# Kernel tuning notes

Measured on AMD Instinct MI355X. Metric: run time of the kernel, lower is better.

## Reference

```python
import jax, jax.numpy as jnp
import numpy as np

B, S, F, D, H, L, NSUB, DFF = 64, 128, 62, 256, 4, 6, 32, 512
DH = D // 2           # each attention branch works on half of d_model
DEPTH = DH // H       # per-head dim = 32
NEG = -1000000000.0


def _rescale(w):
    # (1+e) / (1+exp(1-w))
    e1 = jnp.exp(jnp.float32(1.0))
    return (1.0 + e1) / (1.0 + jnp.exp(1.0 - w))


def _ln(x, g, b):
    mu = jnp.mean(x, -1, keepdims=True)
    v = jnp.var(x, -1, keepdims=True)
    return (x - mu) / jnp.sqrt(v + 1e-6) * g + b


def _heads(x, W, b):
    bsz, s, _ = x.shape
    return (x @ W + b).reshape(bsz, s, H, DEPTH).transpose(0, 2, 1, 3)  # (B,H,S,depth)


def setup_inputs():
    key = jax.random.key(0)
    ks = list(jax.random.split(key, 16))
    it = iter(ks)
    n = lambda shape: jax.random.normal(next(it), shape, jnp.float32) * 0.02
    inp = {
        "x": jax.random.normal(next(it), (B, S, F), jnp.float32),
        "adj_matrix": jax.random.normal(next(it), (B, S, S), jnp.float32),
        "dist_matrix": jax.random.uniform(next(it), (B, S, S), jnp.float32) * 10.0,
        "atom_match_matrix": jax.random.uniform(next(it), (B, NSUB, S), jnp.float32),
        "sum_atoms": jnp.ones((B, NSUB, 1), jnp.float32),
        "emb_W": n((F, D)), "emb_b": jnp.zeros((D,), jnp.float32),
        "glob_W": n((D, D)), "glob_b": jnp.zeros((D,), jnp.float32),
    }
    # per-layer params, stacked along leading L axis for lax.scan
    for p in ["Wq1", "Wk1", "Wv1", "Wo1", "Wq2", "Wk2", "Wv2", "Wo2"]:
        inp[p] = n((L, DH, DH))
    for p in ["bq1", "bk1", "bv1", "bo1", "bq2", "bk2", "bv2", "bo2"]:
        inp[p] = jnp.zeros((L, DH), jnp.float32)
    inp["Wf1"] = n((L, D, DFF)); inp["bf1"] = jnp.zeros((L, DFF), jnp.float32)
    inp["Wf2"] = n((L, DFF, D)); inp["bf2"] = jnp.zeros((L, D), jnp.float32)
    inp["g1"] = jnp.ones((L, D), jnp.float32); inp["be1"] = jnp.zeros((L, D), jnp.float32)
    inp["g2"] = jnp.ones((L, D), jnp.float32); inp["be2"] = jnp.zeros((L, D), jnp.float32)
    return inp


def reference(x, adj_matrix, dist_matrix, atom_match_matrix, sum_atoms,
              emb_W, emb_b, glob_W, glob_b,
              Wq1, Wk1, Wv1, Wo1, Wq2, Wk2, Wv2, Wo2,
              bq1, bk1, bv1, bo1, bq2, bk2, bv2, bo2,
              Wf1, bf1, Wf2, bf2, g1, be1, g2, be2):
    # padding mask from raw atom features: (B,1,1,S)
    mask = (jnp.sum(x, -1) == 0).astype(jnp.float32)[:, None, None, :]
    adj = adj_matrix[:, None]                  # (B,1,S,S) additive bias
    dist = _rescale(dist_matrix)[:, None]      # (B,1,S,S) multiplicative bias
    scale = 1.0 / jnp.sqrt(jnp.float32(DEPTH))

    h = jax.nn.relu(x @ emb_W + emb_b)         # embedding (eval mode, no dropout)

    def layer(h, p):
        (wq1, wk1, wv1, wo1, wq2, wk2, wv2, wo2,
         bq1_, bk1_, bv1_, bo1_, bq2_, bk2_, bv2_, bo2_,
         wf1, bf1_, wf2, bf2_, gg1, bb1, gg2, bb2) = p
        x1, x2 = jnp.split(h, 2, axis=-1)
        # local branch: plain scaled dot product + mask + adjacency bias
        Q = _heads(x1, wq1, bq1_); K = _heads(x1, wk1, bk1_); V = _heads(x1, wv1, bv1_)
        s = jnp.einsum('bhid,bhjd->bhij', Q, K) * scale + mask * NEG + adj
        o = jnp.einsum('bhij,bhjd->bhid', jax.nn.softmax(s, -1), V)
        x_l = o.transpose(0, 2, 1, 3).reshape(h.shape[0], S, DH) @ wo1 + bo1_
        # global branch: relu(QK^T) * rescaled_dist * scale + mask
        Q = _heads(x2, wq2, bq2_); K = _heads(x2, wk2, bk2_); V = _heads(x2, wv2, bv2_)
        s = jax.nn.relu(jnp.einsum('bhid,bhjd->bhij', Q, K)) * dist * scale + mask * NEG
        o = jnp.einsum('bhij,bhjd->bhid', jax.nn.softmax(s, -1), V)
        x_g = o.transpose(0, 2, 1, 3).reshape(h.shape[0], S, DH) @ wo2 + bo2_
        attn = jnp.concatenate([x_l, x_g], -1)
        out1 = _ln(h + attn, gg1, bb1)
        ffn = jax.nn.gelu(out1 @ wf1 + bf1_, approximate=False) @ wf2 + bf2_
        return _ln(ffn + out1, gg2, bb2), None

    xs = (Wq1, Wk1, Wv1, Wo1, Wq2, Wk2, Wv2, Wo2,
          bq1, bk1, bv1, bo1, bq2, bk2, bv2, bo2,
          Wf1, bf1, Wf2, bf2, g1, be1, g2, be2)
    h, _ = jax.lax.scan(layer, h, xs)

    pooled = (atom_match_matrix @ h) / sum_atoms      # (B,NSUB,D)
    out = jax.nn.relu(pooled @ glob_W + glob_b)
    return out
```

## Files before the change

kernel.cpp:

```cpp
#include <hip/hip_runtime.h>
#include <math.h>

#define B_ 64
#define S_ 128
#define F_ 62
#define D_ 256
#define H_ 4
#define L_ 6
#define NSUB_ 32
#define DFF_ 512
#define DH_ 128
#define DEPTH_ 32
#define MS_ (B_*S_)
#define NEGV (-1000000000.0f)
#define SCALE_ 0.17677669529663687f

typedef unsigned short u16;
typedef __attribute__((ext_vector_type(8))) short short8;
typedef __attribute__((ext_vector_type(4))) float f32x4;

__device__ __forceinline__ u16 f2b(float f){
  unsigned u = __float_as_uint(f);
  unsigned r = (u + 0x7fffu + ((u >> 16) & 1u)) >> 16;
  return (u16)r;
}

__device__ __forceinline__ void glds16(const void* g, void* l){
  __builtin_amdgcn_global_load_lds(
      (const __attribute__((address_space(1))) unsigned int*)g,
      (__attribute__((address_space(3))) unsigned int*)l, 16, 0, 0);
}

__global__ __launch_bounds__(256) void adjrescale_kernel(
    const float* __restrict__ adj, const float* __restrict__ dist,
    const float* __restrict__ maskb,
    float* __restrict__ adjm, float* __restrict__ distr){
  size_t i = (size_t)blockIdx.x*256 + threadIdx.x;
  int j = (int)(i & (S_-1));
  int b = (int)(i >> 14);
  const float e1 = 2.718281828459045f;
  distr[i] = (1.0f + e1) / (1.0f + expf(1.0f - dist[i])) * SCALE_;
  adjm[i]  = adj[i] + maskb[b*S_ + j];
}

struct TD { const float* src; u16* dst; int K, N, L; };
struct TDs { TD d[11]; };
__global__ __launch_bounds__(256) void transpose_all_kernel(TDs a){
  const TD p = a.d[blockIdx.z];
  int n0 = blockIdx.x*32, k0 = blockIdx.y*32;
  if(n0 >= p.N || k0 >= p.K) return;
  __shared__ float tbuf[32][33];
  int tx = threadIdx.x, ty = threadIdx.y;
  for(int l = 0; l < p.L; l++){
    const float* src = p.src + (size_t)l*p.K*p.N;
    u16* dst = p.dst + (size_t)l*p.K*p.N;
    #pragma unroll
    for(int i = 0; i < 4; i++)
      tbuf[ty + i*8][tx] = src[(size_t)(k0 + ty + i*8)*p.N + n0 + tx];
    __syncthreads();
    #pragma unroll
    for(int i = 0; i < 4; i++)
      dst[(size_t)(n0 + ty + i*8)*p.K + k0 + tx] = f2b(tbuf[tx][ty + i*8]);
    __syncthreads();
  }
}

__global__ __launch_bounds__(256) void embed_kernel(const float* __restrict__ x,
    const float* __restrict__ W, const float* __restrict__ bias,
    float* __restrict__ h, u16* __restrict__ h_bf, float* __restrict__ maskb){
  __shared__ float xs[4][F_];
  int r0 = blockIdx.x*4;
  int t = threadIdx.x;
  if(t < 4*F_){ int rr = t / F_, ff = t - rr*F_; xs[rr][ff] = x[(size_t)(r0+rr)*F_ + ff]; }
  __syncthreads();
  if(t < 4){
    float s = 0.f;
    #pragma unroll
    for(int f = 0; f < F_; f++) s += xs[t][f];
    maskb[r0 + t] = (s == 0.0f) ? NEGV : 0.0f;
  }
  float b = bias[t];
  float a0=b, a1=b, a2=b, a3=b;
  for(int k=0; k<F_; k++){
    float w = W[k*D_ + t];
    a0 = fmaf(xs[0][k], w, a0);
    a1 = fmaf(xs[1][k], w, a1);
    a2 = fmaf(xs[2][k], w, a2);
    a3 = fmaf(xs[3][k], w, a3);
  }
  a0 = fmaxf(a0, 0.f); a1 = fmaxf(a1, 0.f); a2 = fmaxf(a2, 0.f); a3 = fmaxf(a3, 0.f);
  h[(size_t)(r0+0)*D_ + t] = a0;  h_bf[(size_t)(r0+0)*D_ + t] = f2b(a0);
  h[(size_t)(r0+1)*D_ + t] = a1;  h_bf[(size_t)(r0+1)*D_ + t] = f2b(a1);
  h[(size_t)(r0+2)*D_ + t] = a2;  h_bf[(size_t)(r0+2)*D_ + t] = f2b(a2);
  h[(size_t)(r0+3)*D_ + t] = a3;  h_bf[(size_t)(r0+3)*D_ + t] = f2b(a3);
}

struct MG {
  const u16* A; const u16* W; const float* bias; void* C;
  int lda, K, ldc, aofs, cofs;
};
struct MG6 { MG g[6]; };

template<int TM, bool OUTBF, int ACT>
__global__ __launch_bounds__(256) void mgemm_kernel(MG6 args){
  const MG p = args.g[blockIdx.z];
  __shared__ u16 As[TM*32];
  __shared__ u16 Bs[128*32];
  const int t    = threadIdx.x;
  const int lane = t & 63;
  const int w    = t >> 6;
  const int ln   = lane & 15;
  const int qd   = lane >> 4;
  const int mw   = (w & 1) * (TM/2);
  const int nw   = (w >> 1) * 64;
  const int m0   = blockIdx.x * TM;
  const int n0   = blockIdx.y * 128;
  constexpr int MI = TM/32;
  f32x4 acc[MI][4];
  #pragma unroll
  for(int i=0;i<MI;i++)
    #pragma unroll
    for(int j=0;j<4;j++) acc[i][j] = (f32x4){0.f,0.f,0.f,0.f};

  const int srow = t >> 2;
  const int sc8  = (t & 3) * 8;

  for(int k0 = 0; k0 < p.K; k0 += 32){
    __syncthreads();
    glds16(p.A + (size_t)(m0 + srow)*p.lda + p.aofs + k0 + sc8, As + t*8);
    if(TM == 128)
      glds16(p.A + (size_t)(m0 + 64 + srow)*p.lda + p.aofs + k0 + sc8, As + (t+256)*8);
    glds16(p.W + (size_t)(n0 + srow)*p.K + k0 + sc8, Bs + t*8);
    glds16(p.W + (size_t)(n0 + 64 + srow)*p.K + k0 + sc8, Bs + (t+256)*8);
    __syncthreads();

    short8 a[MI], b[4];
    #pragma unroll
    for(int i=0;i<MI;i++) a[i] = *(const short8*)&As[(mw + i*16 + ln)*32 + qd*8];
    #pragma unroll
    for(int j=0;j<4;j++)  b[j] = *(const short8*)&Bs[(nw + j*16 + ln)*32 + qd*8];
    #pragma unroll
    for(int i=0;i<MI;i++)
      #pragma unroll
      for(int j=0;j<4;j++)
        acc[i][j] = __builtin_amdgcn_mfma_f32_16x16x32_bf16(a[i], b[j], acc[i][j], 0, 0, 0);
  }

  #pragma unroll
  for(int i=0;i<MI;i++){
    #pragma unroll
    for(int j=0;j<4;j++){
      int col = n0 + nw + j*16 + ln;
      float bv = p.bias[col];
      int rowb = m0 + mw + i*16 + qd*4;
      #pragma unroll
      for(int r=0;r<4;r++){
        float v = acc[i][j][r] + bv;
        if(ACT == 1) v = fmaxf(v, 0.f);
        if(ACT == 2) v = 0.5f*v*(1.0f + erff(v*0.70710678118654752f));
        size_t idx = (size_t)(rowb + r)*p.ldc + p.cofs + col;
        if(OUTBF) ((u16*)p.C)[idx] = f2b(v);
        else      ((float*)p.C)[idx] = v;
      }
    }
  }
}

struct QAArgs { const u16 *wq, *wk, *wv; const float *bq, *bk, *bv; };

__global__ __launch_bounds__(256) void qkv_attn_kernel(
    const u16* __restrict__ h_bf,
    QAArgs a1, QAArgs a2,
    const float* __restrict__ adjm, const float* __restrict__ distr,
    const float* __restrict__ maskb,
    u16* __restrict__ o1, u16* __restrict__ o2)
{
  __shared__ u16 SH[21760];
  u16* As = SH;
  u16* Bs = SH + 4096;
  u16* Qs = SH + 7168;
  u16* Ks = SH + 12288;
  u16* Vt = SH + 17408;
  u16* Ps = SH;

  const int bh = blockIdx.x;
  const int b  = bh >> 2;
  const int hh = bh & 3;
  const int branch = blockIdx.y;
  const QAArgs qa = branch ? a2 : a1;
  const u16* wqp = qa.wq + (size_t)hh*32*DH_;
  const u16* wkp = qa.wk + (size_t)hh*32*DH_;
  const u16* wvp = qa.wv + (size_t)hh*32*DH_;
  const int t = threadIdx.x;
  const int w = t >> 6, lane = t & 63;
  const int ln = lane & 15, qd = lane >> 4;
  const size_t rowbase = (size_t)b * S_;
  const int srow = t >> 2, sc8 = (t & 3) * 8;

  f32x4 acc[2][6];
  #pragma unroll
  for(int i=0;i<2;i++)
    #pragma unroll
    for(int j=0;j<6;j++) acc[i][j] = (f32x4){0.f,0.f,0.f,0.f};

  for(int k0 = 0; k0 < DH_; k0 += 32){
    __syncthreads();
    glds16(h_bf + (rowbase + srow)*D_ + branch*DH_ + k0 + sc8, As + t*8);
    glds16(h_bf + (rowbase + 64 + srow)*D_ + branch*DH_ + k0 + sc8, As + (t+256)*8);
    {
      int r = t >> 2;
      const u16* wp = (r < 32) ? wqp : wkp;
      glds16(wp + (size_t)(r & 31)*DH_ + k0 + sc8, Bs + t*8);
    }
    if(t < 128){
      int c = 256 + t;
      glds16(wvp + (size_t)((c>>2) - 64)*DH_ + k0 + (c&3)*8, Bs + c*8);
    }
    __syncthreads();
    short8 av[2];
    #pragma unroll
    for(int mt = 0; mt < 2; mt++)
      av[mt] = *(const short8*)&As[(w*32 + mt*16 + ln)*32 + qd*8];
    #pragma unroll
    for(int nt = 0; nt < 6; nt++){
      short8 bv = *(const short8*)&Bs[(nt*16 + ln)*32 + qd*8];
      #pragma unroll
      for(int mt = 0; mt < 2; mt++)
        acc[mt][nt] = __builtin_amdgcn_mfma_f32_16x16x32_bf16(av[mt], bv, acc[mt][nt], 0, 0, 0);
    }
  }

  {
    const float* bqp = qa.bq + hh*32;
    const float* bkp = qa.bk + hh*32;
    const float* bvp = qa.bv + hh*32;
    #pragma unroll
    for(int mt = 0; mt < 2; mt++){
      int rb = w*32 + mt*16 + qd*4;
      #pragma unroll
      for(int j = 0; j < 2; j++){
        int d = j*16 + ln;
        float bq_ = bqp[d], bk_ = bkp[d], bv_ = bvp[d];
        #pragma unroll
        for(int r = 0; r < 4; r++){
          Qs[(rb+r)*40 + d]   = f2b(acc[mt][j][r]   + bq_);
          Ks[(rb+r)*40 + d]   = f2b(acc[mt][2+j][r] + bk_);
          Vt[d*136 + rb + r]  = f2b(acc[mt][4+j][r] + bv_);
        }
      }
    }
  }
  __syncthreads();

  const int mbase = w * 32;
  short8 qf[2];
  #pragma unroll
  for(int mt = 0; mt < 2; mt++)
    qf[mt] = *(const short8*)&Qs[(mbase + mt*16 + ln)*40 + qd*8];
  short8 kf[8];
  #pragma unroll
  for(int nt = 0; nt < 8; nt++)
    kf[nt] = *(const short8*)&Ks[(nt*16 + ln)*40 + qd*8];
  __syncthreads();

  f32x4 sc[2][8];
  #pragma unroll
  for(int mt = 0; mt < 2; mt++)
    #pragma unroll
    for(int nt = 0; nt < 8; nt++)
      sc[mt][nt] = __builtin_amdgcn_mfma_f32_16x16x32_bf16(
          qf[mt], kf[nt], (f32x4){0.f,0.f,0.f,0.f}, 0, 0, 0);

  float mskv[8];
  if(branch){
    #pragma unroll
    for(int nt = 0; nt < 8; nt++) mskv[nt] = maskb[rowbase + nt*16 + ln];
  }

  #pragma unroll
  for(int mt = 0; mt < 2; mt++){
    #pragma unroll
    for(int r = 0; r < 4; r++){
      int row = mbase + mt*16 + qd*4 + r;
      const float* arow = (branch ? distr : adjm) + (rowbase + row)*S_ + ln;
      #pragma unroll
      for(int nt = 0; nt < 8; nt++){
        float g = arow[nt*16];
        float v;
        if(branch == 0) v = sc[mt][nt][r]*SCALE_ + g;
        else            v = fmaxf(sc[mt][nt][r], 0.f)*g + mskv[nt];
        sc[mt][nt][r] = v;
      }
    }
  }

  #pragma unroll
  for(int mt = 0; mt < 2; mt++){
    #pragma unroll
    for(int r = 0; r < 4; r++){
      float m = -3.4e38f;
      #pragma unroll
      for(int nt = 0; nt < 8; nt++) m = fmaxf(m, sc[mt][nt][r]);
      m = fmaxf(m, __shfl_xor(m, 1));
      m = fmaxf(m, __shfl_xor(m, 2));
      m = fmaxf(m, __shfl_xor(m, 4));
      m = fmaxf(m, __shfl_xor(m, 8));
      float sum = 0.f;
      float e[8];
      #pragma unroll
      for(int nt = 0; nt < 8; nt++){ e[nt] = __expf(sc[mt][nt][r] - m); sum += e[nt]; }
      sum += __shfl_xor(sum, 1);
      sum += __shfl_xor(sum, 2);
      sum += __shfl_xor(sum, 4);
      sum += __shfl_xor(sum, 8);
      float inv = 1.0f / sum;
      int row = mbase + mt*16 + qd*4 + r;
      #pragma unroll
      for(int nt = 0; nt < 8; nt++) Ps[row*136 + nt*16 + ln] = f2b(e[nt] * inv);
    }
  }

  f32x4 oacc[2][2];
  #pragma unroll
  for(int mt = 0; mt < 2; mt++)
    #pragma unroll
    for(int n2 = 0; n2 < 2; n2++) oacc[mt][n2] = (f32x4){0.f,0.f,0.f,0.f};
  #pragma unroll
  for(int kk = 0; kk < 4; kk++){
    short8 pa[2], vb[2];
    #pragma unroll
    for(int mt = 0; mt < 2; mt++)
      pa[mt] = *(const short8*)&Ps[(mbase + mt*16 + ln)*136 + kk*32 + qd*8];
    #pragma unroll
    for(int n2 = 0; n2 < 2; n2++)
      vb[n2] = *(const short8*)&Vt[(n2*16 + ln)*136 + kk*32 + qd*8];
    #pragma unroll
    for(int mt = 0; mt < 2; mt++)
      #pragma unroll
      for(int n2 = 0; n2 < 2; n2++)
        oacc[mt][n2] = __builtin_amdgcn_mfma_f32_16x16x32_bf16(pa[mt], vb[n2], oacc[mt][n2], 0, 0, 0);
  }

  u16* Og = branch ? o2 : o1;
  #pragma unroll
  for(int mt = 0; mt < 2; mt++){
    #pragma unroll
    for(int n2 = 0; n2 < 2; n2++){
      #pragma unroll
      for(int r = 0; r < 4; r++){
        int row = mbase + mt*16 + qd*4 + r;
        int d   = n2*16 + ln;
        Og[(rowbase + row)*DH_ + hh*DEPTH_ + d] = f2b(oacc[mt][n2][r]);
      }
    }
  }
}

__global__ __launch_bounds__(128) void oproj_ln_kernel(
    const u16* __restrict__ o1, const u16* __restrict__ o2,
    const u16* __restrict__ w1, const u16* __restrict__ w2,
    const float* __restrict__ b1, const float* __restrict__ b2,
    const float* __restrict__ hres,
    const float* __restrict__ g, const float* __restrict__ be,
    float* __restrict__ out, u16* __restrict__ outb)
{
  __shared__ u16 As1[32*32], As2[32*32], Bs1[128*32], Bs2[128*32];
  __shared__ float biasv[256], gs[256], bes[256];
  const int t = threadIdx.x;
  const int lane = t & 63, w = t >> 6;
  const int ln = lane & 15, qd = lane >> 4;
  const int m0 = blockIdx.x * 32;
  biasv[t] = b1[t & 127]; biasv[128 + t] = b2[t & 127];
  gs[t] = g[t]; gs[128+t] = g[128+t];
  bes[t] = be[t]; bes[128+t] = be[128+t];
  const int sc8 = (t & 3) * 8;
  f32x4 acc[16];
  #pragma unroll
  for(int i=0;i<16;i++) acc[i] = (f32x4){0.f,0.f,0.f,0.f};

  for(int k0 = 0; k0 < DH_; k0 += 32){
    __syncthreads();
    glds16(o1 + (size_t)(m0 + (t>>2))*DH_ + k0 + sc8, As1 + t*8);
    glds16(o2 + (size_t)(m0 + (t>>2))*DH_ + k0 + sc8, As2 + t*8);
    #pragma unroll
    for(int j = 0; j < 4; j++){
      int c = t + 128*j;
      glds16(w1 + (size_t)(c>>2)*DH_ + k0 + sc8, Bs1 + c*8);
      glds16(w2 + (size_t)(c>>2)*DH_ + k0 + sc8, Bs2 + c*8);
    }
    __syncthreads();
    short8 a1 = *(const short8*)&As1[(w*16+ln)*32 + qd*8];
    short8 a2 = *(const short8*)&As2[(w*16+ln)*32 + qd*8];
    #pragma unroll
    for(int nt = 0; nt < 8; nt++){
      short8 bv = *(const short8*)&Bs1[(nt*16+ln)*32 + qd*8];
      acc[nt] = __builtin_amdgcn_mfma_f32_16x16x32_bf16(a1, bv, acc[nt], 0, 0, 0);
    }
    #pragma unroll
    for(int nt = 0; nt < 8; nt++){
      short8 bv = *(const short8*)&Bs2[(nt*16+ln)*32 + qd*8];
      acc[8+nt] = __builtin_amdgcn_mfma_f32_16x16x32_bf16(a2, bv, acc[8+nt], 0, 0, 0);
    }
  }

  const int rb = m0 + w*16 + qd*4;
  float mu[4] = {0,0,0,0};
  #pragma unroll
  for(int nt = 0; nt < 16; nt++){
    int col = nt*16 + ln;
    float bv = biasv[col];
    #pragma unroll
    for(int r = 0; r < 4; r++){
      float v = acc[nt][r] + bv + hres[(size_t)(rb+r)*D_ + col];
      acc[nt][r] = v;
      mu[r] += v;
    }
  }
  #pragma unroll
  for(int r = 0; r < 4; r++){
    float s = mu[r];
    s += __shfl_xor(s,1); s += __shfl_xor(s,2); s += __shfl_xor(s,4); s += __shfl_xor(s,8);
    mu[r] = s * (1.0f/D_);
  }
  float iv[4] = {0,0,0,0};
  #pragma unroll
  for(int nt = 0; nt < 16; nt++)
    #pragma unroll
    for(int r = 0; r < 4; r++){ float d = acc[nt][r] - mu[r]; iv[r] += d*d; }
  #pragma unroll
  for(int r = 0; r < 4; r++){
    float s = iv[r];
    s += __shfl_xor(s,1); s += __shfl_xor(s,2); s += __shfl_xor(s,4); s += __shfl_xor(s,8);
    iv[r] = rsqrtf(s*(1.0f/D_) + 1e-6f);
  }
  #pragma unroll
  for(int nt = 0; nt < 16; nt++){
    int col = nt*16 + ln;
    float gg = gs[col], bb = bes[col];
    #pragma unroll
    for(int r = 0; r < 4; r++){
      float y = (acc[nt][r] - mu[r])*iv[r]*gg + bb;
      size_t idx = (size_t)(rb+r)*D_ + col;
      out[idx] = y;
      outb[idx] = f2b(y);
    }
  }
}

__global__ __launch_bounds__(128) void ffn2_ln_kernel(
    const u16* __restrict__ A, const u16* __restrict__ W,
    const float* __restrict__ bias,
    const float* __restrict__ res,
    const float* __restrict__ g, const float* __restrict__ be,
    float* __restrict__ out, u16* __restrict__ outb)
{
  __shared__ u16 As[32*32], Bs[256*32];
  __shared__ float biasv[256], gs[256], bes[256];
  const int t = threadIdx.x;
  const int lane = t & 63, w = t >> 6;
  const int ln = lane & 15, qd = lane >> 4;
  const int m0 = blockIdx.x * 32;
  biasv[t] = bias[t]; biasv[128+t] = bias[128+t];
  gs[t] = g[t]; gs[128+t] = g[128+t];
  bes[t] = be[t]; bes[128+t] = be[128+t];
  const int sc8 = (t & 3) * 8;
  f32x4 acc[16];
  #pragma unroll
  for(int i=0;i<16;i++) acc[i] = (f32x4){0.f,0.f,0.f,0.f};

  for(int k0 = 0; k0 < DFF_; k0 += 32){
    __syncthreads();
    glds16(A + (size_t)(m0 + (t>>2))*DFF_ + k0 + sc8, As + t*8);
    #pragma unroll
    for(int j = 0; j < 8; j++){
      int c = t + 128*j;
      glds16(W + (size_t)(c>>2)*DFF_ + k0 + sc8, Bs + c*8);
    }
    __syncthreads();
    short8 a = *(const short8*)&As[(w*16+ln)*32 + qd*8];
    #pragma unroll
    for(int nt = 0; nt < 16; nt++){
      short8 bv = *(const short8*)&Bs[(nt*16+ln)*32 + qd*8];
      acc[nt] = __builtin_amdgcn_mfma_f32_16x16x32_bf16(a, bv, acc[nt], 0, 0, 0);
    }
  }

  const int rb = m0 + w*16 + qd*4;
  float mu[4] = {0,0,0,0};
  #pragma unroll
  for(int nt = 0; nt < 16; nt++){
    int col = nt*16 + ln;
    float bv = biasv[col];
    #pragma unroll
    for(int r = 0; r < 4; r++){
      float v = acc[nt][r] + bv + res[(size_t)(rb+r)*D_ + col];
      acc[nt][r] = v;
      mu[r] += v;
    }
  }
  #pragma unroll
  for(int r = 0; r < 4; r++){
    float s = mu[r];
    s += __shfl_xor(s,1); s += __shfl_xor(s,2); s += __shfl_xor(s,4); s += __shfl_xor(s,8);
    mu[r] = s * (1.0f/D_);
  }
  float iv[4] = {0,0,0,0};
  #pragma unroll
  for(int nt = 0; nt < 16; nt++)
    #pragma unroll
    for(int r = 0; r < 4; r++){ float d = acc[nt][r] - mu[r]; iv[r] += d*d; }
  #pragma unroll
  for(int r = 0; r < 4; r++){
    float s = iv[r];
    s += __shfl_xor(s,1); s += __shfl_xor(s,2); s += __shfl_xor(s,4); s += __shfl_xor(s,8);
    iv[r] = rsqrtf(s*(1.0f/D_) + 1e-6f);
  }
  #pragma unroll
  for(int nt = 0; nt < 16; nt++){
    int col = nt*16 + ln;
    float gg = gs[col], bb = bes[col];
    #pragma unroll
    for(int r = 0; r < 4; r++){
      float y = (acc[nt][r] - mu[r])*iv[r]*gg + bb;
      size_t idx = (size_t)(rb+r)*D_ + col;
      out[idx] = y;
      outb[idx] = f2b(y);
    }
  }
}

__global__ __launch_bounds__(256) void pool_kernel(
    const float* __restrict__ amm, const float* __restrict__ sum_atoms,
    const float* __restrict__ h, u16* __restrict__ pooled_bf)
{
  __shared__ float as[S_];
  int bn = blockIdx.x;
  int b  = bn >> 5;
  int t  = threadIdx.x;
  if(t < S_) as[t] = amm[(size_t)bn*S_ + t];
  __syncthreads();
  float acc = 0.f;
  const float* hb = h + (size_t)b*S_*D_ + t;
  #pragma unroll 4
  for(int s = 0; s < S_; s++) acc = fmaf(as[s], hb[(size_t)s*D_], acc);
  pooled_bf[(size_t)bn*D_ + t] = f2b(acc / sum_atoms[bn]);
}

extern "C" void kernel_launch(void* const* d_in, const int* in_sizes, int n_in,
                              void* d_out, int out_size, void* d_ws, size_t ws_size,
                              hipStream_t stream)
{
  const float* x     = (const float*)d_in[0];
  const float* adj   = (const float*)d_in[1];
  const float* dist  = (const float*)d_in[2];
  const float* amm   = (const float*)d_in[3];
  const float* sum_a = (const float*)d_in[4];
  const float* embW  = (const float*)d_in[5];
  const float* embB  = (const float*)d_in[6];
  const float* globW = (const float*)d_in[7];
  const float* globB = (const float*)d_in[8];
  const float* Wq1 = (const float*)d_in[9],  *Wk1 = (const float*)d_in[10],
             *Wv1 = (const float*)d_in[11], *Wo1 = (const float*)d_in[12],
             *Wq2 = (const float*)d_in[13], *Wk2 = (const float*)d_in[14],
             *Wv2 = (const float*)d_in[15], *Wo2 = (const float*)d_in[16];
  const float* bq1 = (const float*)d_in[17], *bk1 = (const float*)d_in[18],
             *bv1 = (const float*)d_in[19], *bo1 = (const float*)d_in[20],
             *bq2 = (const float*)d_in[21], *bk2 = (const float*)d_in[22],
             *bv2 = (const float*)d_in[23], *bo2 = (const float*)d_in[24];
  const float* Wf1 = (const float*)d_in[25], *bf1 = (const float*)d_in[26],
             *Wf2 = (const float*)d_in[27], *bf2 = (const float*)d_in[28],
             *g1  = (const float*)d_in[29], *be1 = (const float*)d_in[30],
             *g2  = (const float*)d_in[31], *be2 = (const float*)d_in[32];

  float* wsf = (float*)d_ws;
  float* h     = wsf; wsf += (size_t)MS_*D_;
  float* maskb = wsf; wsf += MS_;
  float* distr = wsf; wsf += (size_t)B_*S_*S_;
  float* adjm  = wsf; wsf += (size_t)B_*S_*S_;
  float* slab  = wsf; wsf += (size_t)MS_*DH_*8;
  float* out1  = wsf; wsf += (size_t)MS_*D_;
  u16* bb = (u16*)wsf;
  u16* h_bf    = bb; bb += (size_t)MS_*D_;
  u16* out1_bf = bb; bb += (size_t)MS_*D_;
  u16* pooled_bf = bb; bb += (size_t)B_*NSUB_*D_;
  u16* globWt  = bb; bb += (size_t)D_*D_;
  u16* wq1t = bb; bb += (size_t)L_*DH_*DH_;
  u16* wk1t = bb; bb += (size_t)L_*DH_*DH_;
  u16* wv1t = bb; bb += (size_t)L_*DH_*DH_;
  u16* wo1t = bb; bb += (size_t)L_*DH_*DH_;
  u16* wq2t = bb; bb += (size_t)L_*DH_*DH_;
  u16* wk2t = bb; bb += (size_t)L_*DH_*DH_;
  u16* wv2t = bb; bb += (size_t)L_*DH_*DH_;
  u16* wo2t = bb; bb += (size_t)L_*DH_*DH_;
  u16* wf1t = bb; bb += (size_t)L_*D_*DFF_;
  u16* wf2t = bb; bb += (size_t)L_*DFF_*D_;
  u16* ffn1_bf = (u16*)slab;
  u16* o1_bf   = (u16*)slab + (size_t)MS_*DH_*6;
  u16* o2_bf   = (u16*)slab + (size_t)MS_*DH_*7;

  embed_kernel<<<MS_/4, 256, 0, stream>>>(x, embW, embB, h, h_bf, maskb);
  adjrescale_kernel<<<(B_*S_*S_)/256, 256, 0, stream>>>(adj, dist, maskb, adjm, distr);
  {
    TDs td;
    const float* S8[8] = {Wq1, Wk1, Wv1, Wo1, Wq2, Wk2, Wv2, Wo2};
    u16* D8[8] = {wq1t, wk1t, wv1t, wo1t, wq2t, wk2t, wv2t, wo2t};
    for(int i = 0; i < 8; i++) td.d[i] = {S8[i], D8[i], DH_, DH_, L_};
    td.d[8]  = {Wf1, wf1t, D_, DFF_, L_};
    td.d[9]  = {Wf2, wf2t, DFF_, D_, L_};
    td.d[10] = {globW, globWt, D_, D_, 1};
    transpose_all_kernel<<<dim3(16,16,11), dim3(32,8), 0, stream>>>(td);
  }

  for(int l = 0; l < L_; l++){
    QAArgs a1 = { wq1t + (size_t)l*DH_*DH_, wk1t + (size_t)l*DH_*DH_, wv1t + (size_t)l*DH_*DH_,
                  bq1 + (size_t)l*DH_, bk1 + (size_t)l*DH_, bv1 + (size_t)l*DH_ };
    QAArgs a2 = { wq2t + (size_t)l*DH_*DH_, wk2t + (size_t)l*DH_*DH_, wv2t + (size_t)l*DH_*DH_,
                  bq2 + (size_t)l*DH_, bk2 + (size_t)l*DH_, bv2 + (size_t)l*DH_ };
    qkv_attn_kernel<<<dim3(B_*H_, 2), 256, 0, stream>>>(h_bf, a1, a2, adjm, distr, maskb,
                                                        o1_bf, o2_bf);
    oproj_ln_kernel<<<MS_/32, 128, 0, stream>>>(
        o1_bf, o2_bf,
        wo1t + (size_t)l*DH_*DH_, wo2t + (size_t)l*DH_*DH_,
        bo1 + (size_t)l*DH_, bo2 + (size_t)l*DH_,
        h, g1 + (size_t)l*D_, be1 + (size_t)l*D_,
        out1, out1_bf);
    {
      MG6 a;
      a.g[0].A = out1_bf; a.g[0].W = wf1t + (size_t)l*D_*DFF_;
      a.g[0].bias = bf1 + (size_t)l*DFF_; a.g[0].C = ffn1_bf;
      a.g[0].lda = D_; a.g[0].K = D_; a.g[0].ldc = DFF_;
      a.g[0].aofs = 0; a.g[0].cofs = 0;
      mgemm_kernel<64,true,2><<<dim3(MS_/64, DFF_/128, 1), 256, 0, stream>>>(a);
    }
    ffn2_ln_kernel<<<MS_/32, 128, 0, stream>>>(
        ffn1_bf, wf2t + (size_t)l*DFF_*D_,
        bf2 + (size_t)l*D_,
        out1, g2 + (size_t)l*D_, be2 + (size_t)l*D_,
        h, h_bf);
  }

  pool_kernel<<<B_*NSUB_, 256, 0, stream>>>(amm, sum_a, h, pooled_bf);
  {
    MG6 a;
    a.g[0].A = pooled_bf; a.g[0].W = globWt;
    a.g[0].bias = globB; a.g[0].C = (float*)d_out;
    a.g[0].lda = D_; a.g[0].K = D_; a.g[0].ldc = D_;
    a.g[0].aofs = 0; a.g[0].cofs = 0;
    mgemm_kernel<64,false,1><<<dim3((B_*NSUB_)/64, D_/128, 1), 256, 0, stream>>>(a);
  }
}
```

Baseline: 475.1 us.

## Fuse output projection, LN1, FFN1+GELU, FFN2 and LN2 into one tail kernel

Replaces the per-layer oproj_ln, FFN1 GEMM and ffn2_ln launches with a single 256-thread kernel per 32-row tile. The LN1 output and GELU intermediate stay in shared memory instead of round-tripping through global buffers. Weights are now read straight from global memory as MFMA fragments rather than staged through LDS. Each block now rereads the full FFN weights, and LayerNorm switches to a one-pass sum/sum-of-squares variance, which is slightly less numerically robust.

```diff
diff --git a/kernel.cpp b/kernel.cpp
--- a/kernel.cpp
+++ b/kernel.cpp
@@ -356,175 +356,223 @@
   }
 }
 
-__global__ __launch_bounds__(128) void oproj_ln_kernel(
-    const u16* __restrict__ o1, const u16* __restrict__ o2,
-    const u16* __restrict__ w1, const u16* __restrict__ w2,
-    const float* __restrict__ b1, const float* __restrict__ b2,
-    const float* __restrict__ hres,
-    const float* __restrict__ g, const float* __restrict__ be,
-    float* __restrict__ out, u16* __restrict__ outb)
-{
-  __shared__ u16 As1[32*32], As2[32*32], Bs1[128*32], Bs2[128*32];
-  __shared__ float biasv[256], gs[256], bes[256];
+struct TailArgs {
+  const u16 *o1, *o2, *wo1, *wo2, *w1, *w2;
+  const float *bo1, *bo2, *bf1, *bf2, *g1, *be1, *g2, *be2;
+  float *h; u16 *h_bf;
+};
+
+__global__ __launch_bounds__(256) void tail_kernel(TailArgs p){
+  __shared__ u16 X1[32*264];
+  __shared__ u16 X2[32*520];
+  __shared__ float redS[4][32], redQ[4][32];
   const int t = threadIdx.x;
-  const int lane = t & 63, w = t >> 6;
+  const int w = t >> 6, lane = t & 63;
   const int ln = lane & 15, qd = lane >> 4;
   const int m0 = blockIdx.x * 32;
-  biasv[t] = b1[t & 127]; biasv[128 + t] = b2[t & 127];
-  gs[t] = g[t]; gs[128+t] = g[128+t];
-  bes[t] = be[t]; bes[128+t] = be[128+t];
-  const int sc8 = (t & 3) * 8;
-  f32x4 acc[16];
-  #pragma unroll
-  for(int i=0;i<16;i++) acc[i] = (f32x4){0.f,0.f,0.f,0.f};
-
+  const int branch = w >> 1;
+  const int c0 = w * 64;
+  const int bc0 = (w & 1) * 64;
+
+  const u16* Ao = branch ? p.o2 : p.o1;
+  const u16* Wo = branch ? p.wo2 : p.wo1;
+  const float* bo = branch ? p.bo2 : p.bo1;
+  f32x4 y[2][4];
+  #pragma unroll
+  for(int mt=0;mt<2;mt++)
+    #pragma unroll
+    for(int nt=0;nt<4;nt++) y[mt][nt] = (f32x4){0.f,0.f,0.f,0.f};
+
+  #pragma unroll
   for(int k0 = 0; k0 < DH_; k0 += 32){
-    __syncthreads();
-    glds16(o1 + (size_t)(m0 + (t>>2))*DH_ + k0 + sc8, As1 + t*8);
-    glds16(o2 + (size_t)(m0 + (t>>2))*DH_ + k0 + sc8, As2 + t*8);
-    #pragma unroll
-    for(int j = 0; j < 4; j++){
-      int c = t + 128*j;
-      glds16(w1 + (size_t)(c>>2)*DH_ + k0 + sc8, Bs1 + c*8);
-      glds16(w2 + (size_t)(c>>2)*DH_ + k0 + sc8, Bs2 + c*8);
-    }
-    __syncthreads();
-    short8 a1 = *(const short8*)&As1[(w*16+ln)*32 + qd*8];
-    short8 a2 = *(const short8*)&As2[(w*16+ln)*32 + qd*8];
-    #pragma unroll
-    for(int nt = 0; nt < 8; nt++){
-      short8 bv = *(const short8*)&Bs1[(nt*16+ln)*32 + qd*8];
-      acc[nt] = __builtin_amdgcn_mfma_f32_16x16x32_bf16(a1, bv, acc[nt], 0, 0, 0);
-    }
-    #pragma unroll
-    for(int nt = 0; nt < 8; nt++){
-      short8 bv = *(const short8*)&Bs2[(nt*16+ln)*32 + qd*8];
-      acc[8+nt] = __builtin_amdgcn_mfma_f32_16x16x32_bf16(a2, bv, acc[8+nt], 0, 0, 0);
-    }
-  }
-
-  const int rb = m0 + w*16 + qd*4;
-  float mu[4] = {0,0,0,0};
-  #pragma unroll
-  for(int nt = 0; nt < 16; nt++){
-    int col = nt*16 + ln;
-    float bv = biasv[col];
-    #pragma unroll
-    for(int r = 0; r < 4; r++){
-      float v = acc[nt][r] + bv + hres[(size_t)(rb+r)*D_ + col];
-      acc[nt][r] = v;
-      mu[r] += v;
-    }
-  }
-  #pragma unroll
-  for(int r = 0; r < 4; r++){
-    float s = mu[r];
-    s += __shfl_xor(s,1); s += __shfl_xor(s,2); s += __shfl_xor(s,4); s += __shfl_xor(s,8);
-    mu[r] = s * (1.0f/D_);
-  }
-  float iv[4] = {0,0,0,0};
-  #pragma unroll
-  for(int nt = 0; nt < 16; nt++)
-    #pragma unroll
-    for(int r = 0; r < 4; r++){ float d = acc[nt][r] - mu[r]; iv[r] += d*d; }
-  #pragma unroll
-  for(int r = 0; r < 4; r++){
-    float s = iv[r];
-    s += __shfl_xor(s,1); s += __shfl_xor(s,2); s += __shfl_xor(s,4); s += __shfl_xor(s,8);
-    iv[r] = rsqrtf(s*(1.0f/D_) + 1e-6f);
-  }
-  #pragma unroll
-  for(int nt = 0; nt < 16; nt++){
-    int col = nt*16 + ln;
-    float gg = gs[col], bb = bes[col];
-    #pragma unroll
-    for(int r = 0; r < 4; r++){
-      float y = (acc[nt][r] - mu[r])*iv[r]*gg + bb;
-      size_t idx = (size_t)(rb+r)*D_ + col;
-      out[idx] = y;
-      outb[idx] = f2b(y);
-    }
-  }
-}
-
-__global__ __launch_bounds__(128) void ffn2_ln_kernel(
-    const u16* __restrict__ A, const u16* __restrict__ W,
-    const float* __restrict__ bias,
-    const float* __restrict__ res,
-    const float* __restrict__ g, const float* __restrict__ be,
-    float* __restrict__ out, u16* __restrict__ outb)
-{
-  __shared__ u16 As[32*32], Bs[256*32];
-  __shared__ float biasv[256], gs[256], bes[256];
-  const int t = threadIdx.x;
-  const int lane = t & 63, w = t >> 6;
-  const int ln = lane & 15, qd = lane >> 4;
-  const int m0 = blockIdx.x * 32;
-  biasv[t] = bias[t]; biasv[128+t] = bias[128+t];
-  gs[t] = g[t]; gs[128+t] = g[128+t];
-  bes[t] = be[t]; bes[128+t] = be[128+t];
-  const int sc8 = (t & 3) * 8;
-  f32x4 acc[16];
-  #pragma unroll
-  for(int i=0;i<16;i++) acc[i] = (f32x4){0.f,0.f,0.f,0.f};
-
+    short8 af[2], bf[4];
+    #pragma unroll
+    for(int mt=0;mt<2;mt++)
+      af[mt] = *(const short8*)(Ao + (size_t)(m0+mt*16+ln)*DH_ + k0 + qd*8);
+    #pragma unroll
+    for(int nt=0;nt<4;nt++)
+      bf[nt] = *(const short8*)(Wo + (size_t)(bc0+nt*16+ln)*DH_ + k0 + qd*8);
+    #pragma unroll
+    for(int mt=0;mt<2;mt++)
+      #pragma unroll
+      for(int nt=0;nt<4;nt++)
+        y[mt][nt] = __builtin_amdgcn_mfma_f32_16x16x32_bf16(af[mt], bf[nt], y[mt][nt], 0, 0, 0);
+  }
+
+  float sS[2][4] = {}, sQ[2][4] = {};
+  #pragma unroll
+  for(int mt=0;mt<2;mt++){
+    #pragma unroll
+    for(int nt=0;nt<4;nt++){
+      int col = c0 + nt*16 + ln;
+      float bv = bo[bc0 + nt*16 + ln];
+      #pragma unroll
+      for(int r=0;r<4;r++){
+        float v = y[mt][nt][r] + bv + p.h[(size_t)(m0+mt*16+qd*4+r)*D_ + col];
+        y[mt][nt][r] = v;
+        sS[mt][r] += v;
+        sQ[mt][r] += v*v;
+      }
+    }
+  }
+  #pragma unroll
+  for(int mt=0;mt<2;mt++)
+    #pragma unroll
+    for(int r=0;r<4;r++){
+      float a = sS[mt][r], b = sQ[mt][r];
+      a += __shfl_xor(a,1); a += __shfl_xor(a,2); a += __shfl_xor(a,4); a += __shfl_xor(a,8);
+      b += __shfl_xor(b,1); b += __shfl_xor(b,2); b += __shfl_xor(b,4); b += __shfl_xor(b,8);
+      sS[mt][r] = a; sQ[mt][r] = b;
+    }
+  if(ln == 0){
+    #pragma unroll
+    for(int mt=0;mt<2;mt++)
+      #pragma unroll
+      for(int r=0;r<4;r++){
+        int row = mt*16 + qd*4 + r;
+        redS[w][row] = sS[mt][r];
+        redQ[w][row] = sQ[mt][r];
+      }
+  }
+  __syncthreads();
+  float mu[2][4], iv[2][4];
+  #pragma unroll
+  for(int mt=0;mt<2;mt++)
+    #pragma unroll
+    for(int r=0;r<4;r++){
+      int row = mt*16 + qd*4 + r;
+      float s = redS[0][row] + redS[1][row] + redS[2][row] + redS[3][row];
+      float q = redQ[0][row] + redQ[1][row] + redQ[2][row] + redQ[3][row];
+      float m_ = s * (1.0f/D_);
+      mu[mt][r] = m_;
+      iv[mt][r] = rsqrtf(q*(1.0f/D_) - m_*m_ + 1e-6f);
+    }
+  #pragma unroll
+  for(int mt=0;mt<2;mt++){
+    #pragma unroll
+    for(int nt=0;nt<4;nt++){
+      int col = c0 + nt*16 + ln;
+      float gg = p.g1[col], bb = p.be1[col];
+      #pragma unroll
+      for(int r=0;r<4;r++){
+        float yy = (y[mt][nt][r] - mu[mt][r]) * iv[mt][r] * gg + bb;
+        y[mt][nt][r] = yy;
+        X1[(mt*16+qd*4+r)*264 + col] = f2b(yy);
+      }
+    }
+  }
+  __syncthreads();
+
+  {
+    const int fc0 = w * 128;
+    f32x4 f1[2][8];
+    #pragma unroll
+    for(int mt=0;mt<2;mt++)
+      #pragma unroll
+      for(int nt=0;nt<8;nt++) f1[mt][nt] = (f32x4){0.f,0.f,0.f,0.f};
+    for(int k0 = 0; k0 < D_; k0 += 32){
+      short8 a0 = *(const short8*)&X1[(ln)*264 + k0 + qd*8];
+      short8 a1 = *(const short8*)&X1[(16+ln)*264 + k0 + qd*8];
+      #pragma unroll
+      for(int nt=0;nt<8;nt++){
+        short8 bfr = *(const short8*)(p.w1 + (size_t)(fc0+nt*16+ln)*D_ + k0 + qd*8);
+        f1[0][nt] = __builtin_amdgcn_mfma_f32_16x16x32_bf16(a0, bfr, f1[0][nt], 0, 0, 0);
+        f1[1][nt] = __builtin_amdgcn_mfma_f32_16x16x32_bf16(a1, bfr, f1[1][nt], 0, 0, 0);
+      }
+    }
+    #pragma unroll
+    for(int mt=0;mt<2;mt++){
+      #pragma unroll
+      for(int nt=0;nt<8;nt++){
+        int col = fc0 + nt*16 + ln;
+        float bv = p.bf1[col];
+        #pragma unroll
+        for(int r=0;r<4;r++){
+          float v = f1[mt][nt][r] + bv;
+          v = 0.5f*v*(1.0f + erff(v*0.70710678118654752f));
+          X2[(mt*16+qd*4+r)*520 + col] = f2b(v);
+        }
+      }
+    }
+  }
+  __syncthreads();
+
+  f32x4 f2[2][4];
+  #pragma unroll
+  for(int mt=0;mt<2;mt++)
+    #pragma unroll
+    for(int nt=0;nt<4;nt++) f2[mt][nt] = (f32x4){0.f,0.f,0.f,0.f};
   for(int k0 = 0; k0 < DFF_; k0 += 32){
-    __syncthreads();
-    glds16(A + (size_t)(m0 + (t>>2))*DFF_ + k0 + sc8, As + t*8);
-    #pragma unroll
-    for(int j = 0; j < 8; j++){
-      int c = t + 128*j;
-      glds16(W + (size_t)(c>>2)*DFF_ + k0 + sc8, Bs + c*8);
-    }
-    __syncthreads();
-    short8 a = *(const short8*)&As[(w*16+ln)*32 + qd*8];
-    #pragma unroll
-    for(int nt = 0; nt < 16; nt++){
-      short8 bv = *(const short8*)&Bs[(nt*16+ln)*32 + qd*8];
-      acc[nt] = __builtin_amdgcn_mfma_f32_16x16x32_bf16(a, bv, acc[nt], 0, 0, 0);
-    }
-  }
-
-  const int rb = m0 + w*16 + qd*4;
-  float mu[4] = {0,0,0,0};
-  #pragma unroll
-  for(int nt = 0; nt < 16; nt++){
-    int col = nt*16 + ln;
-    float bv = biasv[col];
-    #pragma unroll
-    for(int r = 0; r < 4; r++){
-      float v = acc[nt][r] + bv + res[(size_t)(rb+r)*D_ + col];
-      acc[nt][r] = v;
-      mu[r] += v;
-    }
-  }
-  #pragma unroll
-  for(int r = 0; r < 4; r++){
-    float s = mu[r];
-    s += __shfl_xor(s,1); s += __shfl_xor(s,2); s += __shfl_xor(s,4); s += __shfl_xor(s,8);
-    mu[r] = s * (1.0f/D_);
-  }
-  float iv[4] = {0,0,0,0};
-  #pragma unroll
-  for(int nt = 0; nt < 16; nt++)
-    #pragma unroll
-    for(int r = 0; r < 4; r++){ float d = acc[nt][r] - mu[r]; iv[r] += d*d; }
-  #pragma unroll
-  for(int r = 0; r < 4; r++){
-    float s = iv[r];
-    s += __shfl_xor(s,1); s += __shfl_xor(s,2); s += __shfl_xor(s,4); s += __shfl_xor(s,8);
-    iv[r] = rsqrtf(s*(1.0f/D_) + 1e-6f);
-  }
-  #pragma unroll
-  for(int nt = 0; nt < 16; nt++){
-    int col = nt*16 + ln;
-    float gg = gs[col], bb = bes[col];
-    #pragma unroll
-    for(int r = 0; r < 4; r++){
-      float y = (acc[nt][r] - mu[r])*iv[r]*gg + bb;
-      size_t idx = (size_t)(rb+r)*D_ + col;
-      out[idx] = y;
-      outb[idx] = f2b(y);
+    short8 a0 = *(const short8*)&X2[(ln)*520 + k0 + qd*8];
+    short8 a1 = *(const short8*)&X2[(16+ln)*520 + k0 + qd*8];
+    #pragma unroll
+    for(int nt=0;nt<4;nt++){
+      short8 bfr = *(const short8*)(p.w2 + (size_t)(c0+nt*16+ln)*DFF_ + k0 + qd*8);
+      f2[0][nt] = __builtin_amdgcn_mfma_f32_16x16x32_bf16(a0, bfr, f2[0][nt], 0, 0, 0);
+      f2[1][nt] = __builtin_amdgcn_mfma_f32_16x16x32_bf16(a1, bfr, f2[1][nt], 0, 0, 0);
+    }
+  }
+  float sS2[2][4] = {}, sQ2[2][4] = {};
+  #pragma unroll
+  for(int mt=0;mt<2;mt++){
+    #pragma unroll
+    for(int nt=0;nt<4;nt++){
+      int col = c0 + nt*16 + ln;
+      float bv = p.bf2[col];
+      #pragma unroll
+      for(int r=0;r<4;r++){
+        float v = f2[mt][nt][r] + bv + y[mt][nt][r];
+        f2[mt][nt][r] = v;
+        sS2[mt][r] += v;
+        sQ2[mt][r] += v*v;
+      }
+    }
+  }
+  #pragma unroll
+  for(int mt=0;mt<2;mt++)
+    #pragma unroll
+    for(int r=0;r<4;r++){
+      float a = sS2[mt][r], b = sQ2[mt][r];
+      a += __shfl_xor(a,1); a += __shfl_xor(a,2); a += __shfl_xor(a,4); a += __shfl_xor(a,8);
+      b += __shfl_xor(b,1); b += __shfl_xor(b,2); b += __shfl_xor(b,4); b += __shfl_xor(b,8);
+      sS2[mt][r] = a; sQ2[mt][r] = b;
+    }
+  __syncthreads();
+  if(ln == 0){
+    #pragma unroll
+    for(int mt=0;mt<2;mt++)
+      #pragma unroll
+      for(int r=0;r<4;r++){
+        int row = mt*16 + qd*4 + r;
+        redS[w][row] = sS2[mt][r];
+        redQ[w][row] = sQ2[mt][r];
+      }
+  }
+  __syncthreads();
+  #pragma unroll
+  for(int mt=0;mt<2;mt++)
+    #pragma unroll
+    for(int r=0;r<4;r++){
+      int row = mt*16 + qd*4 + r;
+      float s = redS[0][row] + redS[1][row] + redS[2][row] + redS[3][row];
+      float q = redQ[0][row] + redQ[1][row] + redQ[2][row] + redQ[3][row];
+      float m_ = s * (1.0f/D_);
+      mu[mt][r] = m_;
+      iv[mt][r] = rsqrtf(q*(1.0f/D_) - m_*m_ + 1e-6f);
+    }
+  #pragma unroll
+  for(int mt=0;mt<2;mt++){
+    #pragma unroll
+    for(int nt=0;nt<4;nt++){
+      int col = c0 + nt*16 + ln;
+      float gg = p.g2[col], bb = p.be2[col];
+      #pragma unroll
+      for(int r=0;r<4;r++){
+        float yy = (f2[mt][nt][r] - mu[mt][r]) * iv[mt][r] * gg + bb;
+        size_t idx = (size_t)(m0 + mt*16 + qd*4 + r)*D_ + col;
+        p.h[idx] = yy;
+        p.h_bf[idx] = f2b(yy);
+      }
     }
   }
 }
@@ -577,11 +625,9 @@
   float* maskb = wsf; wsf += MS_;
   float* distr = wsf; wsf += (size_t)B_*S_*S_;
   float* adjm  = wsf; wsf += (size_t)B_*S_*S_;
-  float* slab  = wsf; wsf += (size_t)MS_*DH_*8;
-  float* out1  = wsf; wsf += (size_t)MS_*D_;
+  float* slab  = wsf; wsf += (size_t)MS_*DH_;
   u16* bb = (u16*)wsf;
   u16* h_bf    = bb; bb += (size_t)MS_*D_;
-  u16* out1_bf = bb; bb += (size_t)MS_*D_;
   u16* pooled_bf = bb; bb += (size_t)B_*NSUB_*D_;
   u16* globWt  = bb; bb += (size_t)D_*D_;
   u16* wq1t = bb; bb += (size_t)L_*DH_*DH_;
@@ -594,9 +640,8 @@
   u16* wo2t = bb; bb += (size_t)L_*DH_*DH_;
   u16* wf1t = bb; bb += (size_t)L_*D_*DFF_;
   u16* wf2t = bb; bb += (size_t)L_*DFF_*D_;
-  u16* ffn1_bf = (u16*)slab;
-  u16* o1_bf   = (u16*)slab + (size_t)MS_*DH_*6;
-  u16* o2_bf   = (u16*)slab + (size_t)MS_*DH_*7;
+  u16* o1_bf = (u16*)slab;
+  u16* o2_bf = o1_bf + (size_t)MS_*DH_;
 
   embed_kernel<<<MS_/4, 256, 0, stream>>>(x, embW, embB, h, h_bf, maskb);
   adjrescale_kernel<<<(B_*S_*S_)/256, 256, 0, stream>>>(adj, dist, maskb, adjm, distr);
@@ -618,25 +663,16 @@
                   bq2 + (size_t)l*DH_, bk2 + (size_t)l*DH_, bv2 + (size_t)l*DH_ };
     qkv_attn_kernel<<<dim3(B_*H_, 2), 256, 0, stream>>>(h_bf, a1, a2, adjm, distr, maskb,
                                                         o1_bf, o2_bf);
-    oproj_ln_kernel<<<MS_/32, 128, 0, stream>>>(
-        o1_bf, o2_bf,
-        wo1t + (size_t)l*DH_*DH_, wo2t + (size_t)l*DH_*DH_,
-        bo1 + (size_t)l*DH_, bo2 + (size_t)l*DH_,
-        h, g1 + (size_t)l*D_, be1 + (size_t)l*D_,
-        out1, out1_bf);
-    {
-      MG6 a;
-      a.g[0].A = out1_bf; a.g[0].W = wf1t + (size_t)l*D_*DFF_;
-      a.g[0].bias = bf1 + (size_t)l*DFF_; a.g[0].C = ffn1_bf;
-      a.g[0].lda = D_; a.g[0].K = D_; a.g[0].ldc = DFF_;
-      a.g[0].aofs = 0; a.g[0].cofs = 0;
-      mgemm_kernel<64,true,2><<<dim3(MS_/64, DFF_/128, 1), 256, 0, stream>>>(a);
-    }
-    ffn2_ln_kernel<<<MS_/32, 128, 0, stream>>>(
-        ffn1_bf, wf2t + (size_t)l*DFF_*D_,
-        bf2 + (size_t)l*D_,
-        out1, g2 + (size_t)l*D_, be2 + (size_t)l*D_,
-        h, h_bf);
+    TailArgs ta;
+    ta.o1 = o1_bf; ta.o2 = o2_bf;
+    ta.wo1 = wo1t + (size_t)l*DH_*DH_; ta.wo2 = wo2t + (size_t)l*DH_*DH_;
+    ta.w1 = wf1t + (size_t)l*D_*DFF_;  ta.w2 = wf2t + (size_t)l*DFF_*D_;
+    ta.bo1 = bo1 + (size_t)l*DH_; ta.bo2 = bo2 + (size_t)l*DH_;
+    ta.bf1 = bf1 + (size_t)l*DFF_; ta.bf2 = bf2 + (size_t)l*D_;
+    ta.g1 = g1 + (size_t)l*D_; ta.be1 = be1 + (size_t)l*D_;
+    ta.g2 = g2 + (size_t)l*D_; ta.be2 = be2 + (size_t)l*D_;
+    ta.h = h; ta.h_bf = h_bf;
+    tail_kernel<<<MS_/32, 256, 0, stream>>>(ta);
   }
 
   pool_kernel<<<B_*NSUB_, 256, 0, stream>>>(amm, sum_a, h, pooled_bf);
```

New measurement: 453.2 us. 1.05x faster.
